# Performance work log

Hardware: AMD Instinct MI355X
Metric: run time of the kernel (lower is better)

Reference implementation:

```python
import jax, jax.numpy as jnp
import numpy as np

N = 50000      # num_nodes
E = 800000     # num_edges (before self loops)
EMB = 128      # emb_dim
GH = 64        # gcn_hidden
TD = 4         # temporal_dim
B = 64         # batch of sequences
T = 200        # max sequence length
H = 128        # lstm_hidden (per direction)
IN_DIM = 2 + EMB + TD


def lstm_scan(x_tbi, w_ih, w_hh, b_ih, b_hh):
    """x_tbi: [T, B, I] -> hidden states [T, B, H]. PyTorch gate order i,f,g,o."""
    Bsz = x_tbi.shape[1]
    Hh = w_hh.shape[1]

    def step(carry, xt):
        h, c = carry
        g = xt @ w_ih.T + h @ w_hh.T + b_ih + b_hh
        i, f, gg, o = jnp.split(g, 4, axis=-1)
        c = jax.nn.sigmoid(f) * c + jax.nn.sigmoid(i) * jnp.tanh(gg)
        h = jax.nn.sigmoid(o) * jnp.tanh(c)
        return (h, c), h

    init = (jnp.zeros((Bsz, Hh), x_tbi.dtype), jnp.zeros((Bsz, Hh), x_tbi.dtype))
    _, hs = jax.lax.scan(step, init, x_tbi)
    return hs


def gcn_layer(x, W, b, src, dst, ew):
    """PyG GCNConv: linear -> symmetric-norm gather/scatter-add -> bias.
    (self loops already appended to src/dst/ew by caller)"""
    h = x @ W  # [N, out]
    deg = jax.ops.segment_sum(ew, dst, num_segments=N)
    dinv = jnp.where(deg > 0, jax.lax.rsqrt(deg), 0.0)
    norm = dinv[src] * ew * dinv[dst]            # [E+N]
    msg = h[src] * norm[:, None]                  # gather + scale
    return jax.ops.segment_sum(msg, dst, num_segments=N) + b


def setup_inputs() -> dict:
    key = jax.random.key(0)
    ks = jax.random.split(key, 16)
    s = 0.02
    return {
        'x_coords': jax.random.normal(ks[0], (N, 2), jnp.float32),
        'temporal_features': jax.random.uniform(ks[1], (N, TD), jnp.float32, -1.0, 1.0),
        'edge_index': jax.random.randint(ks[2], (2, E), 0, N),
        'edge_weight': jnp.ones((E,), jnp.float32),
        'seq': jax.random.randint(ks[3], (B, T), 0, N),
        'lengths': jax.random.randint(ks[4], (B,), 1, T + 1),
        'node_emb': jax.random.normal(ks[5], (N, EMB), jnp.float32) * s,
        'gcn1_w': jax.random.normal(ks[6], (IN_DIM, GH), jnp.float32) * s,
        'gcn1_b': jnp.zeros((GH,), jnp.float32),
        'gcn2_w': jax.random.normal(ks[7], (GH, EMB), jnp.float32) * s,
        'gcn2_b': jnp.zeros((EMB,), jnp.float32),
        'w_ih_f': jax.random.normal(ks[8], (4 * H, EMB), jnp.float32) * s,
        'w_hh_f': jax.random.normal(ks[9], (4 * H, H), jnp.float32) * s,
        'b_ih_f': jnp.zeros((4 * H,), jnp.float32),
        'b_hh_f': jnp.zeros((4 * H,), jnp.float32),
        'w_ih_b': jax.random.normal(ks[10], (4 * H, EMB), jnp.float32) * s,
        'w_hh_b': jax.random.normal(ks[11], (4 * H, H), jnp.float32) * s,
        'b_ih_b': jnp.zeros((4 * H,), jnp.float32),
        'b_hh_b': jnp.zeros((4 * H,), jnp.float32),
        'attn_w': jax.random.normal(ks[12], (2 * H,), jnp.float32) * s,
        'attn_b': jnp.zeros((), jnp.float32),
        'fc_w': jax.random.normal(ks[13], (2 * H, N), jnp.float32) * s,
        'fc_b': jnp.zeros((N,), jnp.float32),
    }


def reference(x_coords, temporal_features, edge_index, edge_weight, seq, lengths,
              node_emb, gcn1_w, gcn1_b, gcn2_w, gcn2_b,
              w_ih_f, w_hh_f, b_ih_f, b_hh_f,
              w_ih_b, w_hh_b, b_ih_b, b_hh_b,
              attn_w, attn_b, fc_w, fc_b):
    # --- GCN with self loops (PyG add_self_loops=True, fill_value=1) ---
    loop = jnp.arange(N)
    src = jnp.concatenate([edge_index[0], loop])
    dst = jnp.concatenate([edge_index[1], loop])
    ew = jnp.concatenate([edge_weight, jnp.ones((N,), edge_weight.dtype)])

    x = jnp.concatenate([x_coords, node_emb, temporal_features], axis=1)  # [N, 134]
    z = jax.nn.relu(gcn_layer(x, gcn1_w, gcn1_b, src, dst, ew))
    z = gcn_layer(z, gcn2_w, gcn2_b, src, dst, ew)  # dropout = identity (eval)

    # --- sequence embedding + BiLSTM ---
    seq_emb = z[seq]                                  # [B, T, EMB]
    h_f = lstm_scan(seq_emb.transpose(1, 0, 2), w_ih_f, w_hh_f, b_ih_f, b_hh_f)
    h_f = h_f.transpose(1, 0, 2)                      # [B, T, H]

    # backward direction: reverse each sequence within its valid length
    t = jnp.arange(T)
    valid = t[None, :] < lengths[:, None]             # [B, T]
    rev_idx = jnp.where(valid, lengths[:, None] - 1 - t[None, :], t[None, :])
    x_rev = jnp.take_along_axis(seq_emb, rev_idx[:, :, None], axis=1)
    h_b = lstm_scan(x_rev.transpose(1, 0, 2), w_ih_b, w_hh_b, b_ih_b, b_hh_b)
    h_b = jnp.take_along_axis(h_b.transpose(1, 0, 2), rev_idx[:, :, None], axis=1)

    lstm_out = jnp.concatenate([h_f, h_b], axis=-1)   # [B, T, 2H]

    # --- masked attention pooling ---
    scores = lstm_out @ attn_w + attn_b               # [B, T]
    scores = jnp.where(valid, scores, -jnp.inf)
    aw = jax.nn.softmax(scores, axis=1)
    context = jnp.einsum('bt,btd->bd', aw, lstm_out)  # [B, 2H]

    return context @ fc_w + fc_b                      # [B, N]
```

## Files before the change

### kernel.cpp

```cpp
#include <hip/hip_runtime.h>
#include <math.h>

#define NN 50000
#define NE 800000
#define EMB 128
#define GH 64
#define BB 64
#define TT 200
#define HH 128
#define G4 512
#define IND 134
#define PM 128
#define PO 128

__device__ __forceinline__ float sigf(float x) { return 1.0f / (1.0f + __expf(-x)); }
__device__ __forceinline__ float tanhf_(float x) { return 1.0f - 2.0f / (__expf(2.0f * x) + 1.0f); }

__global__ void hist_kernel(const int* __restrict__ ei, const float* __restrict__ ew,
                            int* __restrict__ cnt, float* __restrict__ degw) {
    int e = blockIdx.x * 256 + threadIdx.x;
    if (e >= NE) return;
    int d = ei[NE + e];
    atomicAdd(&cnt[d], 1);
    atomicAdd(&degw[d], ew[e]);
}

__global__ __launch_bounds__(1024) void scan1_kernel(const int* __restrict__ cnt,
                                                     const float* __restrict__ degw,
                                                     float* __restrict__ dinv,
                                                     int* __restrict__ rs, int* __restrict__ partials) {
    __shared__ int s[1024];
    int gid = blockIdx.x * 1024 + threadIdx.x;
    int v = (gid < NN) ? cnt[gid] : 0;
    if (gid < NN) dinv[gid] = rsqrtf(degw[gid] + 1.0f);
    s[threadIdx.x] = v;
    __syncthreads();
    for (int off = 1; off < 1024; off <<= 1) {
        int add = (threadIdx.x >= (unsigned)off) ? s[threadIdx.x - off] : 0;
        __syncthreads();
        s[threadIdx.x] += add;
        __syncthreads();
    }
    if (gid < NN) rs[gid] = s[threadIdx.x] - v;
    if (threadIdx.x == 1023) partials[blockIdx.x] = s[1023];
}

__global__ void misc_kernel(int* __restrict__ partials, int nblk,
                            const float* __restrict__ W1, float* __restrict__ w1t,
                            const float* __restrict__ W2, float* __restrict__ w2t) {
    int blk = blockIdx.x;
    int tid = threadIdx.x;
    if (blk == 0) {
        __shared__ int s[64];
        int v = (tid < nblk) ? partials[tid] : 0;
        s[tid] = v;
        __syncthreads();
        for (int off = 1; off < 64; off <<= 1) {
            int add = (tid >= off) ? s[tid - off] : 0;
            __syncthreads();
            s[tid] += add;
            __syncthreads();
        }
        if (tid < nblk) partials[tid] = s[tid] - v;
    } else if (blk <= 34) {
        int i = (blk - 1) * 256 + tid;
        if (i < 64 * 136) {
            int o = i / 136, j = i - o * 136;
            float v = 0.0f;
            if (j < 128) v = W1[(size_t)(j + 2) * GH + o];
            else if (j < 130) v = W1[(size_t)(j - 128) * GH + o];
            else if (j < 134) v = W1[(size_t)j * GH + o];
            w1t[i] = v;
        }
    } else {
        int i = (blk - 35) * 256 + tid;
        if (i < GH * EMB) {
            int o = i >> 6, k = i & 63;
            w2t[i] = W2[(size_t)k * EMB + o];
        }
    }
}

__global__ __launch_bounds__(1024) void scan3_kernel(const int* __restrict__ partials,
                                                     int* __restrict__ rs, int* __restrict__ cursor) {
    int gid = blockIdx.x * 1024 + threadIdx.x;
    if (gid < NN) {
        int v = rs[gid] + partials[gid >> 10];
        rs[gid] = v;
        cursor[gid] = v;
    }
    if (gid == 0) rs[NN] = NE;
}

__global__ void fill_kernel(const int* __restrict__ ei, const float* __restrict__ ew,
                            const float* __restrict__ dinv, int* __restrict__ cursor,
                            int2* __restrict__ ssrcw) {
    int e = blockIdx.x * 256 + threadIdx.x;
    if (e >= NE) return;
    int s = ei[e], d = ei[NE + e];
    int pos = atomicAdd(&cursor[d], 1);
    ssrcw[pos] = make_int2(s, __float_as_int(ew[e] * dinv[s] * dinv[d]));
}

__global__ __launch_bounds__(256) void gemm1_kernel(const float* __restrict__ coords,
                                                    const float* __restrict__ temporal,
                                                    const float* __restrict__ emb,
                                                    const float* __restrict__ w1t,
                                                    float* __restrict__ h1) {
    __shared__ __align__(16) float xs[128][136];
    __shared__ __align__(16) float wt[64][136];
    int tid = threadIdx.x;
    int m0 = blockIdx.x * 128;
    for (int i = tid; i < 64 * 34; i += 256) {
        int rr = i / 34, w = i - rr * 34;
        float4 v = *(const float4*)&w1t[(size_t)rr * 136 + w * 4];
        int ws = (w < 32) ? (w ^ ((rr >> 3) & 7)) : w;
        *(float4*)&wt[rr][ws * 4] = v;
    }
    for (int i = tid; i < 128 * 32; i += 256) {
        int r = i >> 5, c4 = i & 31;
        int m = m0 + r;
        float4 v = make_float4(0.f, 0.f, 0.f, 0.f);
        if (m < NN) v = *(const float4*)&emb[(size_t)m * EMB + c4 * 4];
        *(float4*)&xs[r][(c4 ^ ((r >> 2) & 7)) * 4] = v;
    }
    for (int i = tid; i < 128 * 8; i += 256) {
        int r = i >> 3, c = i & 7;
        int m = m0 + r;
        float v = 0.0f;
        if (m < NN) {
            if (c < 2) v = coords[2 * m + c];
            else if (c < 6) v = temporal[4 * m + (c - 2)];
        }
        xs[r][128 + c] = v;
    }
    __syncthreads();
    int mt = tid >> 3, ot = tid & 7;
    int xswz = mt & 7, wswz = ot & 7;
    float acc[4][8];
#pragma unroll
    for (int mi = 0; mi < 4; ++mi)
#pragma unroll
        for (int oi = 0; oi < 8; ++oi) acc[mi][oi] = 0.0f;
    for (int k4 = 0; k4 < 34; ++k4) {
        int xk = (k4 < 32) ? (k4 ^ xswz) : k4;
        int wk = (k4 < 32) ? (k4 ^ wswz) : k4;
        float4 xv[4], wv[8];
#pragma unroll
        for (int mi = 0; mi < 4; ++mi) xv[mi] = *(const float4*)&xs[mt * 4 + mi][xk * 4];
#pragma unroll
        for (int oi = 0; oi < 8; ++oi) wv[oi] = *(const float4*)&wt[ot * 8 + oi][wk * 4];
#pragma unroll
        for (int mi = 0; mi < 4; ++mi)
#pragma unroll
            for (int oi = 0; oi < 8; ++oi)
                acc[mi][oi] += xv[mi].x * wv[oi].x + xv[mi].y * wv[oi].y
                             + xv[mi].z * wv[oi].z + xv[mi].w * wv[oi].w;
    }
#pragma unroll
    for (int mi = 0; mi < 4; ++mi) {
        int m = m0 + mt * 4 + mi;
        if (m >= NN) continue;
        int ob = ot * 8;
        *(float4*)&h1[(size_t)m * GH + ob] = make_float4(acc[mi][0], acc[mi][1], acc[mi][2], acc[mi][3]);
        *(float4*)&h1[(size_t)m * GH + ob + 4] = make_float4(acc[mi][4], acc[mi][5], acc[mi][6], acc[mi][7]);
    }
}

__global__ __launch_bounds__(256) void agg_kernel(const float* __restrict__ hin,
                                                  const int* __restrict__ rs,
                                                  const int2* __restrict__ ssrcw,
                                                  const float* __restrict__ dinv,
                                                  const float* __restrict__ bias, int relu,
                                                  float* __restrict__ hout) {
    int lane = threadIdx.x & 63;
    int wid = threadIdx.x >> 6;
    int n = blockIdx.x * 4 + wid;
    if (n >= NN) return;
    float dv = dinv[n];
    float acc = hin[(size_t)n * GH + lane] * (dv * dv);
    int i = rs[n], e1 = rs[n + 1];
    for (; i + 7 < e1; i += 8) {
        int4 p0 = *(const int4*)&ssrcw[i];
        int4 p1 = *(const int4*)&ssrcw[i + 2];
        int4 p2 = *(const int4*)&ssrcw[i + 4];
        int4 p3 = *(const int4*)&ssrcw[i + 6];
        float a0 = hin[(size_t)p0.x * GH + lane];
        float a1 = hin[(size_t)p0.z * GH + lane];
        float a2 = hin[(size_t)p1.x * GH + lane];
        float a3 = hin[(size_t)p1.z * GH + lane];
        float a4 = hin[(size_t)p2.x * GH + lane];
        float a5 = hin[(size_t)p2.z * GH + lane];
        float a6 = hin[(size_t)p3.x * GH + lane];
        float a7 = hin[(size_t)p3.z * GH + lane];
        acc += a0 * __int_as_float(p0.y) + a1 * __int_as_float(p0.w)
             + a2 * __int_as_float(p1.y) + a3 * __int_as_float(p1.w)
             + a4 * __int_as_float(p2.y) + a5 * __int_as_float(p2.w)
             + a6 * __int_as_float(p3.y) + a7 * __int_as_float(p3.w);
    }
    for (; i + 3 < e1; i += 4) {
        int4 p0 = *(const int4*)&ssrcw[i];
        int4 p1 = *(const int4*)&ssrcw[i + 2];
        float a0 = hin[(size_t)p0.x * GH + lane];
        float a1 = hin[(size_t)p0.z * GH + lane];
        float a2 = hin[(size_t)p1.x * GH + lane];
        float a3 = hin[(size_t)p1.z * GH + lane];
        acc += a0 * __int_as_float(p0.y) + a1 * __int_as_float(p0.w)
             + a2 * __int_as_float(p1.y) + a3 * __int_as_float(p1.w);
    }
    for (; i < e1; ++i) {
        int2 p = ssrcw[i];
        acc += hin[(size_t)p.x * GH + lane] * __int_as_float(p.y);
    }
    if (bias) acc += bias[lane];
    if (relu) acc = fmaxf(acc, 0.0f);
    hout[(size_t)n * GH + lane] = acc;
}

__global__ __launch_bounds__(256) void gemm2_kernel(const float* __restrict__ a2,
                                                    const float* __restrict__ w2t,
                                                    const float* __restrict__ b2,
                                                    float* __restrict__ z2) {
    int m0 = blockIdx.x * 128, o0 = blockIdx.y * 64;
    __shared__ __align__(16) float xs[128][64];
    __shared__ __align__(16) float wt[64][64];
    __shared__ float bsh[64];
    int tid = threadIdx.x;
#pragma unroll
    for (int i = 0; i < 8; ++i) {
        int idx = i * 256 + tid;
        int r = idx >> 4, c4 = idx & 15;
        int m = m0 + r;
        float4 v = (m < NN) ? *(const float4*)&a2[(size_t)m * GH + c4 * 4]
                            : make_float4(0.f, 0.f, 0.f, 0.f);
        *(float4*)&xs[r][(c4 ^ ((r >> 2) & 3)) * 4] = v;
    }
#pragma unroll
    for (int i = 0; i < 4; ++i) {
        int idx = i * 256 + tid;
        int r = idx >> 4, c4 = idx & 15;
        float4 v = *(const float4*)&w2t[(size_t)(o0 + r) * GH + c4 * 4];
        *(float4*)&wt[r][(c4 ^ ((r >> 3) & 7)) * 4] = v;
    }
    if (tid < 64) bsh[tid] = b2[o0 + tid];
    __syncthreads();
    int mt = tid >> 3, ot = tid & 7;
    float acc[4][8];
#pragma unroll
    for (int mi = 0; mi < 4; ++mi)
#pragma unroll
        for (int oi = 0; oi < 8; ++oi) acc[mi][oi] = 0.0f;
    for (int k4 = 0; k4 < 16; ++k4) {
        int xc = (k4 ^ (mt & 3)) * 4;
        int wc = (k4 ^ (ot & 7)) * 4;
        float4 xv[4], wv[8];
#pragma unroll
        for (int mi = 0; mi < 4; ++mi) xv[mi] = *(const float4*)&xs[mt * 4 + mi][xc];
#pragma unroll
        for (int oi = 0; oi < 8; ++oi) wv[oi] = *(const float4*)&wt[ot * 8 + oi][wc];
#pragma unroll
        for (int mi = 0; mi < 4; ++mi)
#pragma unroll
            for (int oi = 0; oi < 8; ++oi)
                acc[mi][oi] += xv[mi].x * wv[oi].x + xv[mi].y * wv[oi].y
                             + xv[mi].z * wv[oi].z + xv[mi].w * wv[oi].w;
    }
#pragma unroll
    for (int mi = 0; mi < 4; ++mi) {
        int m = m0 + mt * 4 + mi;
        if (m >= NN) continue;
        int ob = ot * 8;
        float4 oa = make_float4(acc[mi][0] + bsh[ob + 0], acc[mi][1] + bsh[ob + 1],
                                acc[mi][2] + bsh[ob + 2], acc[mi][3] + bsh[ob + 3]);
        float4 obv = make_float4(acc[mi][4] + bsh[ob + 4], acc[mi][5] + bsh[ob + 5],
                                 acc[mi][6] + bsh[ob + 6], acc[mi][7] + bsh[ob + 7]);
        *(float4*)&z2[(size_t)m * EMB + o0 + ob] = oa;
        *(float4*)&z2[(size_t)m * EMB + o0 + ob + 4] = obv;
    }
}

__global__ __launch_bounds__(256) void pregemm_kernel(const float* __restrict__ z2,
                                                      const int* __restrict__ seq,
                                                      const float* __restrict__ w_ih_f,
                                                      const float* __restrict__ w_ih_b,
                                                      const float* __restrict__ b_ih_f,
                                                      const float* __restrict__ b_hh_f,
                                                      const float* __restrict__ b_ih_b,
                                                      const float* __restrict__ b_hh_b,
                                                      const int* __restrict__ lengths,
                                                      float* __restrict__ xpf,
                                                      float* __restrict__ xpb) {
    int dir = blockIdx.z;
    const float* w_ih = dir ? w_ih_b : w_ih_f;
    int o0 = blockIdx.y * PO;
    int m0 = blockIdx.x * PM;
    __shared__ __align__(16) float xs[PM][EMB];
    __shared__ __align__(16) float ws[PO][EMB];
    __shared__ float bsh[PO];
    int tid = threadIdx.x;
#pragma unroll
    for (int i = 0; i < 16; ++i) {
        int idx = i * 256 + tid;
        int row = idx >> 5, c4 = idx & 31;
        float4 v = *(const float4*)&w_ih[(size_t)(o0 + row) * EMB + c4 * 4];
        *(float4*)&ws[row][(c4 ^ ((row >> 3) & 7)) * 4] = v;
    }
    if (tid < PO) bsh[tid] = dir ? (b_ih_b[o0 + tid] + b_hh_b[o0 + tid])
                                 : (b_ih_f[o0 + tid] + b_hh_f[o0 + tid]);
#pragma unroll
    for (int i = 0; i < 16; ++i) {
        int idx = i * 256 + tid;
        int r = idx >> 5, c4 = idx & 31;
        int m = m0 + r;
        int t = m >> 6, b = m & 63;
        int tsrc = t;
        if (dir) { int len = lengths[b]; tsrc = (t < len) ? (len - 1 - t) : t; }
        int node = seq[b * TT + tsrc];
        float4 v = *(const float4*)&z2[(size_t)node * EMB + c4 * 4];
        *(float4*)&xs[r][(c4 ^ ((r >> 3) & 3)) * 4] = v;
    }
    __syncthreads();
    int mt = tid >> 4, ot = tid & 15;
    int mswz = mt & 3, oswz = ot & 7;
    float acc[8][8];
#pragma unroll
    for (int mi = 0; mi < 8; ++mi)
#pragma unroll
        for (int oi = 0; oi < 8; ++oi) acc[mi][oi] = 0.0f;
    for (int k4 = 0; k4 < 32; ++k4) {
        int xk = (k4 ^ mswz) * 4;
        int wk = (k4 ^ oswz) * 4;
        float4 xv[8], wv[8];
#pragma unroll
        for (int mi = 0; mi < 8; ++mi) xv[mi] = *(const float4*)&xs[mt * 8 + mi][xk];
#pragma unroll
        for (int oi = 0; oi < 8; ++oi) wv[oi] = *(const float4*)&ws[ot * 8 + oi][wk];
#pragma unroll
        for (int mi = 0; mi < 8; ++mi)
#pragma unroll
            for (int oi = 0; oi < 8; ++oi)
                acc[mi][oi] += xv[mi].x * wv[oi].x + xv[mi].y * wv[oi].y
                             + xv[mi].z * wv[oi].z + xv[mi].w * wv[oi].w;
    }
    float* xp = dir ? xpb : xpf;
#pragma unroll
    for (int mi = 0; mi < 8; ++mi) {
        int m = m0 + mt * 8 + mi;
        int ob = ot * 8;
        float4 oa = make_float4(acc[mi][0] + bsh[ob + 0], acc[mi][1] + bsh[ob + 1],
                                acc[mi][2] + bsh[ob + 2], acc[mi][3] + bsh[ob + 3]);
        float4 obv = make_float4(acc[mi][4] + bsh[ob + 4], acc[mi][5] + bsh[ob + 5],
                                 acc[mi][6] + bsh[ob + 6], acc[mi][7] + bsh[ob + 7]);
        *(float4*)&xp[(size_t)m * G4 + o0 + ob] = oa;
        *(float4*)&xp[(size_t)m * G4 + o0 + ob + 4] = obv;
    }
}

#define PIN4(v) asm volatile("" : "+v"(v.x), "+v"(v.y), "+v"(v.z), "+v"(v.w))
__global__ __launch_bounds__(1024, 4) void lstm_kernel(const float* __restrict__ xpf,
                                                       const float* __restrict__ xpb,
                                                       const float* __restrict__ w_hh_f,
                                                       const float* __restrict__ w_hh_b,
                                                       const int* __restrict__ lengths,
                                                       float* __restrict__ hfo,
                                                       float* __restrict__ hbo) {
    int chain = blockIdx.x;
    int dir = chain & 1, b = chain >> 1;
    const float* w_hh = dir ? w_hh_b : w_hh_f;
    const float* xp = dir ? xpb : xpf;
    float* ho = dir ? hbo : hfo;
    int tid = threadIdx.x;
    int u = tid & 127;
    int kq = tid >> 7;
    int len = lengths[b];

    float4 W[4][4];
#pragma unroll
    for (int g = 0; g < 4; ++g)
#pragma unroll
        for (int j4 = 0; j4 < 4; ++j4) {
            W[g][j4] = *(const float4*)&w_hh[(size_t)(g * HH + u) * HH + kq * 16 + j4 * 4];
            PIN4(W[g][j4]);
        }

    __shared__ __align__(16) float hl[HH];
    __shared__ __align__(16) float part[8][HH][4];
    if (tid < HH) hl[tid] = 0.0f;
    __syncthreads();

    float cst = 0.0f, hkeep = 0.0f;
    int tprev = -1;
    float x0 = 0.f, x1 = 0.f, x2 = 0.f, x3 = 0.f;
    const float* xpt = xp + (size_t)b * G4 + u;
    if (tid < HH && len > 0) {
        x0 = xpt[0]; x1 = xpt[HH]; x2 = xpt[2 * HH]; x3 = xpt[3 * HH];
    }
    for (int t = 0; t < len; ++t) {
        float n0 = 0.f, n1 = 0.f, n2 = 0.f, n3 = 0.f;
        if (tid < HH) {
            if (tprev >= 0) ho[((size_t)b * TT + tprev) * HH + u] = hkeep;
            if (t + 1 < len) {
                const float* xn = xpt + (size_t)(t + 1) * (BB * G4);
                n0 = xn[0]; n1 = xn[HH]; n2 = xn[2 * HH]; n3 = xn[3 * HH];
            }
        }
        const float4* h4 = (const float4*)&hl[kq * 16];
        float a0 = 0.f, a1 = 0.f, a2 = 0.f, a3 = 0.f;
#pragma unroll
        for (int j4 = 0; j4 < 4; ++j4) {
            float4 hv = h4[j4];
            a0 += W[0][j4].x * hv.x + W[0][j4].y * hv.y + W[0][j4].z * hv.z + W[0][j4].w * hv.w;
            a1 += W[1][j4].x * hv.x + W[1][j4].y * hv.y + W[1][j4].z * hv.z + W[1][j4].w * hv.w;
            a2 += W[2][j4].x * hv.x + W[2][j4].y * hv.y + W[2][j4].z * hv.z + W[2][j4].w * hv.w;
            a3 += W[3][j4].x * hv.x + W[3][j4].y * hv.y + W[3][j4].z * hv.z + W[3][j4].w * hv.w;
        }
        if (kq) *(float4*)&part[kq][u][0] = make_float4(a0, a1, a2, a3);
        __syncthreads();
        if (tid < HH) {
            float s0 = x0 + a0, s1 = x1 + a1, s2 = x2 + a2, s3 = x3 + a3;
#pragma unroll
            for (int q = 1; q < 8; ++q) {
                float4 p = *(const float4*)&part[q][u][0];
                s0 += p.x; s1 += p.y; s2 += p.z; s3 += p.w;
            }
            float gi = sigf(s0), gf = sigf(s1), gg = tanhf_(s2), go = sigf(s3);
            cst = gf * cst + gi * gg;
            float h = go * tanhf_(cst);
            hl[u] = h;
            hkeep = h;
            tprev = dir ? (len - 1 - t) : t;
            x0 = n0; x1 = n1; x2 = n2; x3 = n3;
        }
        __syncthreads();
    }
    if (tid < HH && tprev >= 0) ho[((size_t)b * TT + tprev) * HH + u] = hkeep;
}

__global__ __launch_bounds__(256) void attn_kernel(const float* __restrict__ hf,
                                                   const float* __restrict__ hb,
                                                   const float* __restrict__ attn_w,
                                                   const float* __restrict__ attn_b,
                                                   const int* __restrict__ lengths,
                                                   float* __restrict__ ctx) {
    int b = blockIdx.x;
    int tid = threadIdx.x;
    int len = lengths[b];
    __shared__ __align__(16) float wl[256];
    __shared__ float pl[256];
    __shared__ float red[256];
    wl[tid] = attn_w[tid];
    __syncthreads();
    float sc = -3.0e38f;
    if (tid < len) {
        const float4* rf = (const float4*)(hf + ((size_t)b * TT + tid) * HH);
        const float4* rb = (const float4*)(hb + ((size_t)b * TT + tid) * HH);
        const float4* w4 = (const float4*)wl;
        float s = attn_b[0];
        for (int k4 = 0; k4 < 32; ++k4) {
            float4 a = rf[k4], ww = w4[k4];
            s += a.x * ww.x + a.y * ww.y + a.z * ww.z + a.w * ww.w;
        }
        for (int k4 = 0; k4 < 32; ++k4) {
            float4 a = rb[k4], ww = w4[32 + k4];
            s += a.x * ww.x + a.y * ww.y + a.z * ww.z + a.w * ww.w;
        }
        sc = s;
    }
    red[tid] = sc;
    __syncthreads();
    for (int off = 128; off > 0; off >>= 1) {
        if (tid < off) red[tid] = fmaxf(red[tid], red[tid + off]);
        __syncthreads();
    }
    float mx = red[0];
    __syncthreads();
    float e = (tid < len) ? __expf(sc - mx) : 0.0f;
    red[tid] = e;
    __syncthreads();
    for (int off = 128; off > 0; off >>= 1) {
        if (tid < off) red[tid] += red[tid + off];
        __syncthreads();
    }
    float inv = 1.0f / red[0];
    pl[tid] = e * inv;
    __syncthreads();
    float acc = 0.0f;
    const float* basep = (tid < HH) ? (hf + (size_t)b * TT * HH + tid)
                                    : (hb + (size_t)b * TT * HH + (tid - HH));
#pragma unroll 4
    for (int t = 0; t < len; ++t) acc += pl[t] * basep[(size_t)t * HH];
    ctx[(size_t)b * 256 + tid] = acc;
}

__global__ __launch_bounds__(256) void fc_kernel(const float* __restrict__ ctx,
                                                 const float* __restrict__ fc_w,
                                                 const float* __restrict__ fc_b,
                                                 float* __restrict__ out) {
    __shared__ __align__(16) float cl[64][256];
    for (int i = threadIdx.x; i < 64 * 256 / 4; i += 256)
        ((float4*)cl)[i] = ((const float4*)ctx)[i];
    __syncthreads();
    int lane = threadIdx.x & 63;
    int bq = threadIdx.x >> 6;
    int nb = blockIdx.x * 256 + lane;
    float acc[16][4];
#pragma unroll
    for (int i = 0; i < 16; ++i)
#pragma unroll
        for (int c = 0; c < 4; ++c) acc[i][c] = 0.0f;
    for (int k4 = 0; k4 < 64; ++k4) {
        int k = k4 * 4;
        float w[4][4];
#pragma unroll
        for (int j = 0; j < 4; ++j)
#pragma unroll
            for (int c = 0; c < 4; ++c) {
                int n = nb + c * 64;
                w[j][c] = (n < NN) ? fc_w[(size_t)(k + j) * NN + n] : 0.0f;
            }
#pragma unroll
        for (int i = 0; i < 16; ++i) {
            float4 cv = *(const float4*)&cl[bq * 16 + i][k];
#pragma unroll
            for (int c = 0; c < 4; ++c)
                acc[i][c] += cv.x * w[0][c] + cv.y * w[1][c] + cv.z * w[2][c] + cv.w * w[3][c];
        }
    }
#pragma unroll
    for (int i = 0; i < 16; ++i)
#pragma unroll
        for (int c = 0; c < 4; ++c) {
            int n = nb + c * 64;
            if (n < NN) out[(size_t)(bq * 16 + i) * NN + n] = acc[i][c] + fc_b[n];
        }
}

extern "C" void kernel_launch(void* const* d_in, const int* in_sizes, int n_in,
                              void* d_out, int out_size, void* d_ws, size_t ws_size,
                              hipStream_t stream) {
    const float* x_coords   = (const float*)d_in[0];
    const float* temporal   = (const float*)d_in[1];
    const int*   edge_index = (const int*)d_in[2];
    const float* edge_w     = (const float*)d_in[3];
    const int*   seq        = (const int*)d_in[4];
    const int*   lengths    = (const int*)d_in[5];
    const float* node_emb   = (const float*)d_in[6];
    const float* gcn1_w     = (const float*)d_in[7];
    const float* gcn1_b     = (const float*)d_in[8];
    const float* gcn2_w     = (const float*)d_in[9];
    const float* gcn2_b     = (const float*)d_in[10];
    const float* w_ih_f     = (const float*)d_in[11];
    const float* w_hh_f     = (const float*)d_in[12];
    const float* b_ih_f     = (const float*)d_in[13];
    const float* b_hh_f     = (const float*)d_in[14];
    const float* w_ih_b     = (const float*)d_in[15];
    const float* w_hh_b     = (const float*)d_in[16];
    const float* b_ih_b     = (const float*)d_in[17];
    const float* b_hh_b     = (const float*)d_in[18];
    const float* attn_w     = (const float*)d_in[19];
    const float* attn_b     = (const float*)d_in[20];
    const float* fc_w       = (const float*)d_in[21];
    const float* fc_b       = (const float*)d_in[22];
    float* out = (float*)d_out;

    char* base = (char*)d_ws;
    size_t off = 0;
    auto alloc = [&](size_t nbytes) -> void* {
        void* p = base + off;
        off = (off + nbytes + 255) & ~(size_t)255;
        return p;
    };
    int*   cnt     = (int*)alloc((size_t)2 * NN * 4);
    float* degw    = (float*)(cnt + NN);
    float* dinv    = (float*)alloc((size_t)NN * 4);
    int*   rs      = (int*)alloc(((size_t)NN + 1) * 4);
    int*   cursor  = (int*)alloc((size_t)NN * 4);
    int*   partials= (int*)alloc(64 * 4);
    int2*  ssrcw   = (int2*)alloc((size_t)NE * 8);
    float* h1      = (float*)alloc((size_t)NN * GH * 4);
    float* z1      = (float*)alloc((size_t)NN * GH * 4);
    float* a2      = h1;
    float* w1t     = (float*)alloc((size_t)64 * 136 * 4);
    float* w2t     = (float*)alloc((size_t)GH * EMB * 4);
    float* z2      = (float*)alloc((size_t)NN * EMB * 4);
    float* xpf     = (float*)alloc((size_t)TT * BB * G4 * 4);
    float* xpb     = (float*)alloc((size_t)TT * BB * G4 * 4);
    float* hfo     = (float*)alloc((size_t)BB * TT * HH * 4);
    float* hbo     = (float*)alloc((size_t)BB * TT * HH * 4);
    float* ctx     = (float*)alloc((size_t)BB * 256 * 4);
    (void)ws_size; (void)in_sizes; (void)n_in; (void)out_size;

    hipMemsetAsync(cnt, 0, (size_t)2 * NN * 4, stream);

    hist_kernel<<<(NE + 255) / 256, 256, 0, stream>>>(edge_index, edge_w, cnt, degw);
    const int nblk = (NN + 1023) / 1024;
    scan1_kernel<<<nblk, 1024, 0, stream>>>(cnt, degw, dinv, rs, partials);
    misc_kernel<<<67, 256, 0, stream>>>(partials, nblk, gcn1_w, w1t, gcn2_w, w2t);
    scan3_kernel<<<nblk, 1024, 0, stream>>>(partials, rs, cursor);
    fill_kernel<<<(NE + 255) / 256, 256, 0, stream>>>(edge_index, edge_w, dinv, cursor, ssrcw);

    gemm1_kernel<<<(NN + 127) / 128, 256, 0, stream>>>(x_coords, temporal, node_emb, w1t, h1);
    agg_kernel<<<(NN + 3) / 4, 256, 0, stream>>>(h1, rs, ssrcw, dinv, gcn1_b, 1, z1);
    agg_kernel<<<(NN + 3) / 4, 256, 0, stream>>>(z1, rs, ssrcw, dinv, (const float*)nullptr, 0, a2);
    gemm2_kernel<<<dim3((NN + 127) / 128, 2), 256, 0, stream>>>(a2, w2t, gcn2_b, z2);

    pregemm_kernel<<<dim3(TT * BB / PM, G4 / PO, 2), 256, 0, stream>>>(
        z2, seq, w_ih_f, w_ih_b, b_ih_f, b_hh_f, b_ih_b, b_hh_b, lengths, xpf, xpb);
    lstm_kernel<<<BB * 2, 1024, 0, stream>>>(xpf, xpb, w_hh_f, w_hh_b, lengths, hfo, hbo);
    attn_kernel<<<BB, 256, 0, stream>>>(hfo, hbo, attn_w, attn_b, lengths, ctx);
    fc_kernel<<<(NN + 255) / 256, 256, 0, stream>>>(ctx, fc_w, fc_b, out);
}
```

Baseline: 645.8 us.

## Fold GCN layer-2 weight into LSTM input projection, drop full-graph gemm2

Precomputes W_ih·W2ᵀ and the combined bias (W_ih·b2 + b_ih + b_hh) in a small kernel, so the second GCN linear layer is never applied to all 50k nodes. The pregemm now gathers only the 64-wide aggregated features of the sequence nodes and runs a K=64 instead of K=128 contraction. This removes the gemm2 kernel and the z2 write/read, at the cost of one tiny extra kernel and a slightly different float summation order. The agg kernel also loads its row range as a single int2.

```diff
diff --git a/kernel.cpp b/kernel.cpp
--- a/kernel.cpp
+++ b/kernel.cpp
@@ -46,8 +46,7 @@
 }
 
 __global__ void misc_kernel(int* __restrict__ partials, int nblk,
-                            const float* __restrict__ W1, float* __restrict__ w1t,
-                            const float* __restrict__ W2, float* __restrict__ w2t) {
+                            const float* __restrict__ W1, float* __restrict__ w1t) {
     int blk = blockIdx.x;
     int tid = threadIdx.x;
     if (blk == 0) {
@@ -62,7 +61,7 @@
             __syncthreads();
         }
         if (tid < nblk) partials[tid] = s[tid] - v;
-    } else if (blk <= 34) {
+    } else {
         int i = (blk - 1) * 256 + tid;
         if (i < 64 * 136) {
             int o = i / 136, j = i - o * 136;
@@ -72,12 +71,47 @@
             else if (j < 134) v = W1[(size_t)j * GH + o];
             w1t[i] = v;
         }
-    } else {
-        int i = (blk - 35) * 256 + tid;
-        if (i < GH * EMB) {
-            int o = i >> 6, k = i & 63;
-            w2t[i] = W2[(size_t)k * EMB + o];
-        }
+    }
+}
+
+__global__ __launch_bounds__(256) void wcomb_kernel(const float* __restrict__ w_ih_f,
+                                                    const float* __restrict__ w_ih_b,
+                                                    const float* __restrict__ W2,
+                                                    const float* __restrict__ b2,
+                                                    const float* __restrict__ b_ih_f,
+                                                    const float* __restrict__ b_hh_f,
+                                                    const float* __restrict__ b_ih_b,
+                                                    const float* __restrict__ b_hh_b,
+                                                    float* __restrict__ wcomb,
+                                                    float* __restrict__ bcomb) {
+    int bx = blockIdx.x, tid = threadIdx.x;
+    int dir = bx >> 7, o0 = (bx & 127) * 4;
+    const float* w_ih = dir ? w_ih_b : w_ih_f;
+    __shared__ __align__(16) float w2s[GH][EMB];
+    __shared__ __align__(16) float wihs[4][EMB];
+    __shared__ __align__(16) float b2s[EMB];
+    for (int i = tid; i < GH * EMB / 4; i += 256)
+        ((float4*)w2s)[i] = ((const float4*)W2)[i];
+    for (int i = tid; i < 4 * EMB / 4; i += 256) {
+        int oo = i >> 5, e4 = i & 31;
+        ((float4*)wihs)[i] = *(const float4*)&w_ih[(size_t)(o0 + oo) * EMB + e4 * 4];
+    }
+    if (tid < 32) ((float4*)b2s)[tid] = ((const float4*)b2)[tid];
+    __syncthreads();
+    int oo = tid >> 6, k = tid & 63;
+    float acc = 0.0f;
+#pragma unroll 8
+    for (int e4 = 0; e4 < 32; ++e4) {
+        float4 a = *(const float4*)&wihs[oo][e4 * 4];
+        float4 w = *(const float4*)&w2s[k][e4 * 4];
+        acc += a.x * w.x + a.y * w.y + a.z * w.z + a.w * w.w;
+    }
+    wcomb[((size_t)dir * G4 + o0 + oo) * GH + k] = acc;
+    if (tid < 4) {
+        int o = o0 + tid;
+        float s = dir ? (b_ih_b[o] + b_hh_b[o]) : (b_ih_f[o] + b_hh_f[o]);
+        for (int e = 0; e < EMB; ++e) s += wihs[tid][e] * b2s[e];
+        bcomb[dir * G4 + o] = s;
     }
 }
 
@@ -179,7 +213,8 @@
     if (n >= NN) return;
     float dv = dinv[n];
     float acc = hin[(size_t)n * GH + lane] * (dv * dv);
-    int i = rs[n], e1 = rs[n + 1];
+    int2 range = *(const int2*)&rs[n];
+    int i = range.x, e1 = range.y;
     for (; i + 7 < e1; i += 8) {
         int4 p0 = *(const int4*)&ssrcw[i];
         int4 p1 = *(const int4*)&ssrcw[i + 2];
@@ -217,106 +252,39 @@
     hout[(size_t)n * GH + lane] = acc;
 }
 
-__global__ __launch_bounds__(256) void gemm2_kernel(const float* __restrict__ a2,
-                                                    const float* __restrict__ w2t,
-                                                    const float* __restrict__ b2,
-                                                    float* __restrict__ z2) {
-    int m0 = blockIdx.x * 128, o0 = blockIdx.y * 64;
-    __shared__ __align__(16) float xs[128][64];
-    __shared__ __align__(16) float wt[64][64];
-    __shared__ float bsh[64];
-    int tid = threadIdx.x;
-#pragma unroll
-    for (int i = 0; i < 8; ++i) {
-        int idx = i * 256 + tid;
-        int r = idx >> 4, c4 = idx & 15;
-        int m = m0 + r;
-        float4 v = (m < NN) ? *(const float4*)&a2[(size_t)m * GH + c4 * 4]
-                            : make_float4(0.f, 0.f, 0.f, 0.f);
-        *(float4*)&xs[r][(c4 ^ ((r >> 2) & 3)) * 4] = v;
-    }
-#pragma unroll
-    for (int i = 0; i < 4; ++i) {
-        int idx = i * 256 + tid;
-        int r = idx >> 4, c4 = idx & 15;
-        float4 v = *(const float4*)&w2t[(size_t)(o0 + r) * GH + c4 * 4];
-        *(float4*)&wt[r][(c4 ^ ((r >> 3) & 7)) * 4] = v;
-    }
-    if (tid < 64) bsh[tid] = b2[o0 + tid];
-    __syncthreads();
-    int mt = tid >> 3, ot = tid & 7;
-    float acc[4][8];
-#pragma unroll
-    for (int mi = 0; mi < 4; ++mi)
-#pragma unroll
-        for (int oi = 0; oi < 8; ++oi) acc[mi][oi] = 0.0f;
-    for (int k4 = 0; k4 < 16; ++k4) {
-        int xc = (k4 ^ (mt & 3)) * 4;
-        int wc = (k4 ^ (ot & 7)) * 4;
-        float4 xv[4], wv[8];
-#pragma unroll
-        for (int mi = 0; mi < 4; ++mi) xv[mi] = *(const float4*)&xs[mt * 4 + mi][xc];
-#pragma unroll
-        for (int oi = 0; oi < 8; ++oi) wv[oi] = *(const float4*)&wt[ot * 8 + oi][wc];
-#pragma unroll
-        for (int mi = 0; mi < 4; ++mi)
-#pragma unroll
-            for (int oi = 0; oi < 8; ++oi)
-                acc[mi][oi] += xv[mi].x * wv[oi].x + xv[mi].y * wv[oi].y
-                             + xv[mi].z * wv[oi].z + xv[mi].w * wv[oi].w;
-    }
-#pragma unroll
-    for (int mi = 0; mi < 4; ++mi) {
-        int m = m0 + mt * 4 + mi;
-        if (m >= NN) continue;
-        int ob = ot * 8;
-        float4 oa = make_float4(acc[mi][0] + bsh[ob + 0], acc[mi][1] + bsh[ob + 1],
-                                acc[mi][2] + bsh[ob + 2], acc[mi][3] + bsh[ob + 3]);
-        float4 obv = make_float4(acc[mi][4] + bsh[ob + 4], acc[mi][5] + bsh[ob + 5],
-                                 acc[mi][6] + bsh[ob + 6], acc[mi][7] + bsh[ob + 7]);
-        *(float4*)&z2[(size_t)m * EMB + o0 + ob] = oa;
-        *(float4*)&z2[(size_t)m * EMB + o0 + ob + 4] = obv;
-    }
-}
-
-__global__ __launch_bounds__(256) void pregemm_kernel(const float* __restrict__ z2,
+__global__ __launch_bounds__(256) void pregemm_kernel(const float* __restrict__ a2,
                                                       const int* __restrict__ seq,
-                                                      const float* __restrict__ w_ih_f,
-                                                      const float* __restrict__ w_ih_b,
-                                                      const float* __restrict__ b_ih_f,
-                                                      const float* __restrict__ b_hh_f,
-                                                      const float* __restrict__ b_ih_b,
-                                                      const float* __restrict__ b_hh_b,
+                                                      const float* __restrict__ wcomb,
+                                                      const float* __restrict__ bcomb,
                                                       const int* __restrict__ lengths,
                                                       float* __restrict__ xpf,
                                                       float* __restrict__ xpb) {
     int dir = blockIdx.z;
-    const float* w_ih = dir ? w_ih_b : w_ih_f;
     int o0 = blockIdx.y * PO;
     int m0 = blockIdx.x * PM;
-    __shared__ __align__(16) float xs[PM][EMB];
-    __shared__ __align__(16) float ws[PO][EMB];
+    const float* wc = wcomb + (size_t)dir * G4 * GH;
+    __shared__ __align__(16) float xs[PM][GH];
+    __shared__ __align__(16) float ws[PO][GH];
     __shared__ float bsh[PO];
     int tid = threadIdx.x;
 #pragma unroll
-    for (int i = 0; i < 16; ++i) {
+    for (int i = 0; i < 8; ++i) {
         int idx = i * 256 + tid;
-        int row = idx >> 5, c4 = idx & 31;
-        float4 v = *(const float4*)&w_ih[(size_t)(o0 + row) * EMB + c4 * 4];
+        int row = idx >> 4, c4 = idx & 15;
+        float4 v = *(const float4*)&wc[(size_t)(o0 + row) * GH + c4 * 4];
         *(float4*)&ws[row][(c4 ^ ((row >> 3) & 7)) * 4] = v;
     }
-    if (tid < PO) bsh[tid] = dir ? (b_ih_b[o0 + tid] + b_hh_b[o0 + tid])
-                                 : (b_ih_f[o0 + tid] + b_hh_f[o0 + tid]);
-#pragma unroll
-    for (int i = 0; i < 16; ++i) {
+    if (tid < PO) bsh[tid] = bcomb[dir * G4 + o0 + tid];
+#pragma unroll
+    for (int i = 0; i < 8; ++i) {
         int idx = i * 256 + tid;
-        int r = idx >> 5, c4 = idx & 31;
+        int r = idx >> 4, c4 = idx & 15;
         int m = m0 + r;
         int t = m >> 6, b = m & 63;
         int tsrc = t;
         if (dir) { int len = lengths[b]; tsrc = (t < len) ? (len - 1 - t) : t; }
         int node = seq[b * TT + tsrc];
-        float4 v = *(const float4*)&z2[(size_t)node * EMB + c4 * 4];
+        float4 v = *(const float4*)&a2[(size_t)node * GH + c4 * 4];
         *(float4*)&xs[r][(c4 ^ ((r >> 3) & 3)) * 4] = v;
     }
     __syncthreads();
@@ -327,7 +295,7 @@
     for (int mi = 0; mi < 8; ++mi)
 #pragma unroll
         for (int oi = 0; oi < 8; ++oi) acc[mi][oi] = 0.0f;
-    for (int k4 = 0; k4 < 32; ++k4) {
+    for (int k4 = 0; k4 < 16; ++k4) {
         int xk = (k4 ^ mswz) * 4;
         int wk = (k4 ^ oswz) * 4;
         float4 xv[8], wv[8];
@@ -581,8 +549,8 @@
     float* z1      = (float*)alloc((size_t)NN * GH * 4);
     float* a2      = h1;
     float* w1t     = (float*)alloc((size_t)64 * 136 * 4);
-    float* w2t     = (float*)alloc((size_t)GH * EMB * 4);
-    float* z2      = (float*)alloc((size_t)NN * EMB * 4);
+    float* wcomb   = (float*)alloc((size_t)2 * G4 * GH * 4);
+    float* bcomb   = (float*)alloc((size_t)2 * G4 * 4);
     float* xpf     = (float*)alloc((size_t)TT * BB * G4 * 4);
     float* xpb     = (float*)alloc((size_t)TT * BB * G4 * 4);
     float* hfo     = (float*)alloc((size_t)BB * TT * HH * 4);
@@ -595,17 +563,18 @@
     hist_kernel<<<(NE + 255) / 256, 256, 0, stream>>>(edge_index, edge_w, cnt, degw);
     const int nblk = (NN + 1023) / 1024;
     scan1_kernel<<<nblk, 1024, 0, stream>>>(cnt, degw, dinv, rs, partials);
-    misc_kernel<<<67, 256, 0, stream>>>(partials, nblk, gcn1_w, w1t, gcn2_w, w2t);
+    misc_kernel<<<35, 256, 0, stream>>>(partials, nblk, gcn1_w, w1t);
+    wcomb_kernel<<<256, 256, 0, stream>>>(w_ih_f, w_ih_b, gcn2_w, gcn2_b,
+                                          b_ih_f, b_hh_f, b_ih_b, b_hh_b, wcomb, bcomb);
     scan3_kernel<<<nblk, 1024, 0, stream>>>(partials, rs, cursor);
     fill_kernel<<<(NE + 255) / 256, 256, 0, stream>>>(edge_index, edge_w, dinv, cursor, ssrcw);
 
     gemm1_kernel<<<(NN + 127) / 128, 256, 0, stream>>>(x_coords, temporal, node_emb, w1t, h1);
     agg_kernel<<<(NN + 3) / 4, 256, 0, stream>>>(h1, rs, ssrcw, dinv, gcn1_b, 1, z1);
     agg_kernel<<<(NN + 3) / 4, 256, 0, stream>>>(z1, rs, ssrcw, dinv, (const float*)nullptr, 0, a2);
-    gemm2_kernel<<<dim3((NN + 127) / 128, 2), 256, 0, stream>>>(a2, w2t, gcn2_b, z2);
 
     pregemm_kernel<<<dim3(TT * BB / PM, G4 / PO, 2), 256, 0, stream>>>(
-        z2, seq, w_ih_f, w_ih_b, b_ih_f, b_hh_f, b_ih_b, b_hh_b, lengths, xpf, xpb);
+        a2, seq, wcomb, bcomb, lengths, xpf, xpb);
     lstm_kernel<<<BB * 2, 1024, 0, stream>>>(xpf, xpb, w_hh_f, w_hh_b, lengths, hfo, hbo);
     attn_kernel<<<BB, 256, 0, stream>>>(hfo, hbo, attn_w, attn_b, lengths, ctx);
     fc_kernel<<<(NN + 255) / 256, 256, 0, stream>>>(ctx, fc_w, fc_b, out);
```

Result: faster. 568.7 us (median of 2 runs) (-11.9%).
